# Kernel optimization log

Measured on AMD Instinct MI355X. Metric: run time of the kernel, lower is better.

The kernel has to match this reference:

```python
import jax, jax.numpy as jnp
import numpy as np

N = 50000          # total points (25 clouds x 2000 pts)
C = 64             # feature channels (in == out, no bottleneck)
K_NN = 16          # neighbors kept per dilation branch
DILATIONS = (1, 2, 4)
KMAX = K_NN * max(DILATIONS)   # base kNN graph has k*d_max neighbors per node
B = 25             # number of point clouds
EPS = 1e-16


def setup_inputs() -> dict:
    key = jax.random.key(0)
    ks = jax.random.split(key, 8)
    x = jax.random.normal(ks[0], (N, C), jnp.float32)
    pos = jax.random.normal(ks[1], (N, 3), jnp.float32)
    # kNN-style edge_index [2, N*KMAX]: row0 = source/neighbor j, row1 = center i,
    # KMAX consecutive edges per center node, neighbors restricted to the same cloud.
    pts = N // B
    cloud_base = (jnp.arange(N) // pts) * pts
    src = cloud_base[:, None] + jax.random.randint(ks[2], (N, KMAX), 0, pts)
    dst = jnp.broadcast_to(jnp.arange(N)[:, None], (N, KMAX))
    edge_index = jnp.stack([src.reshape(-1), dst.reshape(-1)]).astype(jnp.int32)
    batch = jnp.repeat(jnp.arange(B), pts).astype(jnp.int32)
    nD = len(DILATIONS)
    s = 1.0 / np.sqrt(C)
    Wv = jax.random.normal(ks[3], (nD, C, C), jnp.float32) * s   # lin (value)
    Wq = jax.random.normal(ks[4], (nD, C, C), jnp.float32) * s   # lin_dst
    Wk = jax.random.normal(ks[5], (nD, C, C), jnp.float32) * s   # lin_src
    Wp = jax.random.normal(ks[6], (nD, 3, C), jnp.float32) * (1.0 / np.sqrt(3.0))  # pos_nn
    bp = jax.random.normal(ks[7], (nD, C), jnp.float32) * 0.01
    return dict(x=x, pos=pos, Wv=Wv, Wq=Wq, Wk=Wk, Wp=Wp, bp=bp,
                edge_index=edge_index, batch=batch)


def _dilated_edges(edge_index, k, d):
    # take every d-th of the first k*d neighbors within each node's block -> k edges/node
    e = edge_index.reshape(2, -1, KMAX)[:, :, : k * d : d]
    return e.reshape(2, -1)


def _segment_softmax(a, seg, n):
    amax = jax.ops.segment_max(a, seg, num_segments=n)
    e = jnp.exp(a - amax[seg])
    s = jax.ops.segment_sum(e, seg, num_segments=n)
    return e / (s[seg] + EPS)


def _pt_conv(x, pos, src, dst, Wv, Wq, Wk, Wp, bp):
    # PyG PointTransformerConv: msg = softmax_i(q_i - k_j + delta_ij) * (v_j + delta_ij)
    n = x.shape[0]
    q = x @ Wq        # [N, C]  (lin_dst)
    kk = x @ Wk       # [N, C]  (lin_src)
    v = x @ Wv        # [N, C]  (lin, value)
    delta = (pos[dst] - pos[src]) @ Wp + bp            # [E, C] positional encoding
    alpha = _segment_softmax(q[dst] - kk[src] + delta, dst, n)
    return jax.ops.segment_sum(alpha * (v[src] + delta), dst, num_segments=n)


def reference(x, pos, Wv, Wq, Wk, Wp, bp, edge_index, batch):
    inputs = x
    res = None
    for i, d in enumerate(DILATIONS):
        e = _dilated_edges(edge_index, K_NN, d)
        h = _pt_conv(x, pos, e[0], e[1], Wv[i], Wq[i], Wk[i], Wp[i], bp[i])
        res = h if res is None else jnp.maximum(res, h)   # stack+max over branches
    # global max pool per cloud, gathered back per node
    pool = jax.ops.segment_max(x, batch, num_segments=B)[batch]
    res = jnp.maximum(res, pool)
    return res + inputs   # residual
```

## Files before the change

### kernel.cpp

```cpp
#include <hip/hip_runtime.h>
#include <math.h>

#define NP 50000
#define CH 64
#define KMAX 64
#define KNN 16
#define NB 25
#define PTS (NP / NB)
#define EPSF 1e-16f
#define NTILES (NP / 16)
#define ATILES (NP / 4)
#define L2E 1.4426950408889634f
#define LN2 0.6931471805599453f
#define PPB 8
#define PROWS (PTS / PPB)

typedef __attribute__((ext_vector_type(8))) short short8;
typedef __attribute__((ext_vector_type(4))) float float4v;
typedef __attribute__((ext_vector_type(4))) unsigned int uint4v;
typedef __attribute__((ext_vector_type(2))) unsigned int uint2v;
typedef __attribute__((ext_vector_type(4))) unsigned short ushort4v;

__device__ __forceinline__ ushort f2b(float f) {
  unsigned u = __float_as_uint(f);
  unsigned r = (u + 0x7FFFu + ((u >> 16) & 1u)) >> 16;
  return (ushort)r;
}
__device__ __forceinline__ float b2f(ushort h) {
  return __uint_as_float(((unsigned)h) << 16);
}

#define QBF_BYTES   ((size_t)3 * NP * CH * 2)
#define KVP_BYTES   ((size_t)3 * NP * CH * 4)
#define WPACK_ELEMS (9 * 4 * 2 * 64 * 8)

__global__ __launch_bounds__(256) void prep_kernel(
    const float* __restrict__ x,
    const float* __restrict__ Wv,
    const float* __restrict__ Wq,
    const float* __restrict__ Wk,
    ushort* __restrict__ wpack,
    float* __restrict__ poolP) {
  const int tid = threadIdx.x;
  const int bid = blockIdx.x;
  __shared__ float red[4][CH];

  if (bid < NB * PPB) {
    const int lane = tid & 63;
    const int wave = tid >> 6;
    const int cloud = bid >> 3;
    const int part  = bid & 7;
    const float* xb = x + ((size_t)cloud * PTS + part * PROWS) * CH;
    float m0 = -INFINITY, m1 = -INFINITY;
    for (int r = wave * 2; r < PROWS; r += 8) {
      m0 = fmaxf(m0, xb[(size_t)(r + 0) * CH + lane]);
      m1 = fmaxf(m1, xb[(size_t)(r + 1) * CH + lane]);
    }
    red[wave][lane] = fmaxf(m0, m1);
    __syncthreads();
    if (wave == 0) {
      poolP[(size_t)bid * CH + lane] = fmaxf(fmaxf(red[0][lane], red[1][lane]),
                                             fmaxf(red[2][lane], red[3][lane]));
    }
  } else {
    int pid = (bid - NB * PPB) * 256 + tid;
    if (pid < WPACK_ELEMS) {
      int j     = pid & 7;
      int lane  = (pid >> 3) & 63;
      int kstep = (pid >> 9) & 1;
      int mtile = (pid >> 10) & 3;
      int mat   = pid >> 12;
      const float* W;
      int d;
      float scale;
      if (mat < 3)      { W = Wq; d = mat;     scale = L2E; }
      else if (mat < 6) { W = Wk; d = mat - 3; scale = L2E; }
      else              { W = Wv; d = mat - 6; scale = 1.f; }
      int oc = mtile * 16 + (lane & 15);
      int ic = kstep * 32 + ((lane >> 4) & 3) * 8 + j;
      wpack[pid] = f2b(W[d * CH * CH + ic * CH + oc] * scale);
    }
  }
}

__global__ __launch_bounds__(384) void qkv_mfma(
    const float* __restrict__ x,
    const ushort* __restrict__ wpack,
    ushort* __restrict__ qbf,
    unsigned int* __restrict__ kvp) {
  const int tile = blockIdx.x;
  const int lane = threadIdx.x;
  const int wy   = threadIdx.y;
  const int tid  = wy * 64 + lane;

  __shared__ ushort xs[16 * 64];

  if (tid < 256) {
    int node  = tid >> 4;
    int chunk = tid & 15;
    float4v v = *(const float4v*)(x + ((size_t)(tile * 16 + node)) * CH + chunk * 4);
    ushort4v o;
    o[0] = f2b(v[0]); o[1] = f2b(v[1]); o[2] = f2b(v[2]); o[3] = f2b(v[3]);
    int byte = (chunk * 8) ^ ((node & 7) << 4);
    *(ushort4v*)((char*)xs + node * 128 + byte) = o;
  }
  __syncthreads();

  const int node = lane & 15;
  const int kb2  = (lane >> 4) * 16;
  const char* xrow = (const char*)xs + node * 128;
  const int sw = (node & 7) << 4;
  short8 b0 = *(const short8*)(xrow + (kb2 ^ sw));
  short8 b1 = *(const short8*)(xrow + ((kb2 + 64) ^ sw));
  const int myNode = tile * 16 + node;

  if (wy < 3) {
    const int dd = wy;
    ushort* outQ = qbf + (size_t)dd * NP * CH;
#pragma unroll
    for (int mt = 0; mt < 4; ++mt) {
      short8 a0 = *(const short8*)(wpack +
          ((((size_t)dd * 4 + mt) * 2 + 0) * 64 + lane) * 8);
      short8 a1 = *(const short8*)(wpack +
          ((((size_t)dd * 4 + mt) * 2 + 1) * 64 + lane) * 8);
      float4v acc = {0.f, 0.f, 0.f, 0.f};
      acc = __builtin_amdgcn_mfma_f32_16x16x32_bf16(a0, b0, acc, 0, 0, 0);
      acc = __builtin_amdgcn_mfma_f32_16x16x32_bf16(a1, b1, acc, 0, 0, 0);
      int oc = mt * 16 + (lane >> 4) * 4;
      uint2v o;
      o[0] = (unsigned)f2b(acc[0]) | ((unsigned)f2b(acc[1]) << 16);
      o[1] = (unsigned)f2b(acc[2]) | ((unsigned)f2b(acc[3]) << 16);
      *(uint2v*)(outQ + (size_t)myNode * CH + oc) = o;
    }
  } else {
    const int dd = wy - 3;
    unsigned int* outKV = kvp + (size_t)dd * NP * CH;
#pragma unroll
    for (int mt = 0; mt < 4; ++mt) {
      short8 k0 = *(const short8*)(wpack +
          ((((size_t)(3 + dd) * 4 + mt) * 2 + 0) * 64 + lane) * 8);
      short8 k1 = *(const short8*)(wpack +
          ((((size_t)(3 + dd) * 4 + mt) * 2 + 1) * 64 + lane) * 8);
      short8 v0 = *(const short8*)(wpack +
          ((((size_t)(6 + dd) * 4 + mt) * 2 + 0) * 64 + lane) * 8);
      short8 v1 = *(const short8*)(wpack +
          ((((size_t)(6 + dd) * 4 + mt) * 2 + 1) * 64 + lane) * 8);
      float4v aK = {0.f, 0.f, 0.f, 0.f};
      float4v aV = {0.f, 0.f, 0.f, 0.f};
      aK = __builtin_amdgcn_mfma_f32_16x16x32_bf16(k0, b0, aK, 0, 0, 0);
      aK = __builtin_amdgcn_mfma_f32_16x16x32_bf16(k1, b1, aK, 0, 0, 0);
      aV = __builtin_amdgcn_mfma_f32_16x16x32_bf16(v0, b0, aV, 0, 0, 0);
      aV = __builtin_amdgcn_mfma_f32_16x16x32_bf16(v1, b1, aV, 0, 0, 0);
      int oc = mt * 16 + (lane >> 4) * 4;
      uint4v o;
#pragma unroll
      for (int i = 0; i < 4; ++i)
        o[i] = ((unsigned)f2b(aK[i]) << 16) | (unsigned)f2b(aV[i]);
      *(uint4v*)(outKV + (size_t)myNode * CH + oc) = o;
    }
  }
}

__global__ __launch_bounds__(384, 6) void attn_kernel(
    const float* __restrict__ x,
    const float* __restrict__ pos,
    const float* __restrict__ Wp,
    const float* __restrict__ bp,
    const int*   __restrict__ edge_src,
    const ushort* __restrict__ qbf,
    const unsigned int* __restrict__ kvp,
    const float* __restrict__ poolP,
    float* __restrict__ out) {
  const int bx  = blockIdx.x;
  const int xcd = bx & 7;
  const int kk  = bx >> 3;
  const int base = (ATILES * xcd) >> 3;
  const int cnt  = ((ATILES * (xcd + 1)) >> 3) - base;
  if (kk >= cnt) return;
  const int node0 = (base + kk) * 4;

  const int wy   = threadIdx.y;
  const int dd   = wy % 3;
  const int half = wy / 3;
  const int tid  = wy * 64 + threadIdx.x;

  __shared__ float sEdge[4 * 260];
  __shared__ float sS[6 * 4 * 68];
  __shared__ float sP[6 * 4 * 68];

  if (tid < 256) {
    int nl = tid >> 6, p = tid & 63;
    int nd = node0 + nl;
    int j = edge_src[(size_t)nd * KMAX + p];
    float4v w;
    w[0] = pos[nd * 3 + 0] - pos[j * 3 + 0];
    w[1] = pos[nd * 3 + 1] - pos[j * 3 + 1];
    w[2] = pos[nd * 3 + 2] - pos[j * 3 + 2];
    w[3] = __int_as_float(j << 8);
    *(float4v*)&sEdge[nl * 260 + p * 4] = w;
  }
  __syncthreads();

  const int lane = threadIdx.x;
  const int g    = lane >> 4;
  const int cl   = lane & 15;
  const int node = node0 + g;
  const unsigned clOfs = (unsigned)(cl << 4);

  float4v bq, qorig, wp0, wp1, wp2;
  {
    ushort4v qh = *(const ushort4v*)(qbf + ((size_t)dd * NP + node) * CH + cl * 4);
    const float* WpD = Wp + dd * 192;
    wp0 = *(const float4v*)(WpD + 0 * 64 + cl * 4) * L2E;
    wp1 = *(const float4v*)(WpD + 1 * 64 + cl * 4) * L2E;
    wp2 = *(const float4v*)(WpD + 2 * 64 + cl * 4) * L2E;
    float4v bpv = *(const float4v*)(bp + dd * 64 + cl * 4);
    float4v qf;
#pragma unroll
    for (int i = 0; i < 4; ++i) qf[i] = b2f(qh[i]);
    bq = qf + bpv * L2E;
    qorig = qf * LN2;
  }
  const char* KVb = (const char*)(kvp + (size_t)dd * NP * CH);

  const float* ep = &sEdge[g * 260] + (((half * 8) << dd) * 4);
  const int estep = (1 << dd) * 4;

  float4v s    = {0.f, 0.f, 0.f, 0.f};
  float4v accv = {0.f, 0.f, 0.f, 0.f};
#pragma unroll
  for (int e = 0; e < 8; ++e) {
    float4v w = *(const float4v*)ep;
    ep += estep;
    uint4v u = *(const uint4v*)(KVb + (__float_as_uint(w[3]) + clOfs));
    float4v kf, vf, wgt;
#pragma unroll
    for (int i = 0; i < 4; ++i) kf[i] = __uint_as_float(u[i] & 0xFFFF0000u);
#pragma unroll
    for (int i = 0; i < 4; ++i) vf[i] = __uint_as_float(u[i] << 16);
    float4v t = bq + w[0] * wp0 + w[1] * wp1 + w[2] * wp2;
    float4v a = t - kf;
#pragma unroll
    for (int i = 0; i < 4; ++i) wgt[i] = __builtin_amdgcn_exp2f(a[i]);
    s += wgt;
    accv += wgt * (vf + t * LN2);
  }

  float4v P = accv - qorig * s;
  *(float4v*)&sS[(wy * 4 + g) * 68 + cl * 4] = s;
  *(float4v*)&sP[(wy * 4 + g) * 68 + cl * 4] = P;
  __syncthreads();

  if (wy == 0) {
    float4v res;
#pragma unroll
    for (int d2 = 0; d2 < 3; ++d2) {
      float4v s0 = *(const float4v*)&sS[((d2    ) * 4 + g) * 68 + cl * 4];
      float4v s1 = *(const float4v*)&sS[((d2 + 3) * 4 + g) * 68 + cl * 4];
      float4v p0 = *(const float4v*)&sP[((d2    ) * 4 + g) * 68 + cl * 4];
      float4v p1 = *(const float4v*)&sP[((d2 + 3) * 4 + g) * 68 + cl * 4];
      float4v st = s0 + s1;
      float4v pt = p0 + p1;
      float4v r;
#pragma unroll
      for (int i = 0; i < 4; ++i)
        r[i] = pt[i] * __builtin_amdgcn_rcpf(st[i] + EPSF);
      if (d2 == 0) res = r;
      else {
#pragma unroll
        for (int i = 0; i < 4; ++i) res[i] = fmaxf(res[i], r[i]);
      }
    }
    const int b = node / PTS;
    const float* pp = poolP + (size_t)(b * PPB) * CH + cl * 4;
    float4v pv = *(const float4v*)pp;
#pragma unroll
    for (int q2 = 1; q2 < PPB; ++q2) {
      float4v t2 = *(const float4v*)(pp + (size_t)q2 * CH);
#pragma unroll
      for (int i = 0; i < 4; ++i) pv[i] = fmaxf(pv[i], t2[i]);
    }
    float4v xv = *(const float4v*)(x + (size_t)node * CH + cl * 4);
#pragma unroll
    for (int i = 0; i < 4; ++i) res[i] = fmaxf(res[i], pv[i]) + xv[i];
    *(float4v*)(out + (size_t)node * CH + cl * 4) = res;
  }
}

extern "C" void kernel_launch(void* const* d_in, const int* in_sizes, int n_in,
                              void* d_out, int out_size, void* d_ws, size_t ws_size,
                              hipStream_t stream) {
  const float* x    = (const float*)d_in[0];
  const float* pos  = (const float*)d_in[1];
  const float* Wv   = (const float*)d_in[2];
  const float* Wq   = (const float*)d_in[3];
  const float* Wk   = (const float*)d_in[4];
  const float* Wp   = (const float*)d_in[5];
  const float* bp   = (const float*)d_in[6];
  const int*   ei   = (const int*)d_in[7];
  float* out = (float*)d_out;

  char* wsb = (char*)d_ws;
  ushort* qbf   = (ushort*)wsb;
  unsigned int* kvp = (unsigned int*)(wsb + QBF_BYTES);
  ushort* wpack = (ushort*)(wsb + QBF_BYTES + KVP_BYTES);
  float*  poolP = (float*)(wsb + QBF_BYTES + KVP_BYTES +
                           (size_t)WPACK_ELEMS * 2);

  {
    int packBlocks = (WPACK_ELEMS + 255) / 256;
    dim3 grid(NB * PPB + packBlocks);
    hipLaunchKernelGGL(prep_kernel, grid, dim3(256), 0, stream,
                       x, Wv, Wq, Wk, wpack, poolP);
  }
  {
    dim3 grid(NTILES);
    dim3 block(64, 6);
    hipLaunchKernelGGL(qkv_mfma, grid, block, 0, stream, x, wpack, qbf, kvp);
  }
  {
    dim3 grid(8 * ((ATILES + 7) / 8));
    dim3 block(64, 6);
    hipLaunchKernelGGL(attn_kernel, grid, block, 0, stream,
                       x, pos, Wp, bp, ei, qbf, kvp, poolP, out);
  }
}
```

Measured before the change: 191.1 us.

## Gather only used neighbor edges, prefetch pool/residual early, XCD-remap QKV tiles

The attention kernel now loads only the 48 dilated neighbor edges each node actually uses, instead of all 64, into a compacted shared layout, so the edge-loop reads become contiguous. The pool-max and residual loads move before the first barrier on the finalizing wave (wave 5), so their latency overlaps with the edge gather. The QKV GEMM grid is remapped so that contiguous tiles land on the same XCD, matching the attention kernel. This adds index arithmetic and pads the grid slightly.

```diff
diff --git a/kernel.cpp b/kernel.cpp
--- a/kernel.cpp
+++ b/kernel.cpp
@@ -88,7 +88,14 @@
     const ushort* __restrict__ wpack,
     ushort* __restrict__ qbf,
     unsigned int* __restrict__ kvp) {
-  const int tile = blockIdx.x;
+  const int bx  = blockIdx.x;
+  const int xcd = bx & 7;
+  const int kk  = bx >> 3;
+  const int tbase = (NTILES * xcd) >> 3;
+  const int tcnt  = ((NTILES * (xcd + 1)) >> 3) - tbase;
+  if (kk >= tcnt) return;
+  const int tile = tbase + kk;
+
   const int lane = threadIdx.x;
   const int wy   = threadIdx.y;
   const int tid  = wy * 64 + lane;
@@ -181,32 +188,16 @@
 
   const int wy   = threadIdx.y;
   const int dd   = wy % 3;
-  const int half = wy / 3;
-  const int tid  = wy * 64 + threadIdx.x;
-
-  __shared__ float sEdge[4 * 260];
-  __shared__ float sS[6 * 4 * 68];
-  __shared__ float sP[6 * 4 * 68];
-
-  if (tid < 256) {
-    int nl = tid >> 6, p = tid & 63;
-    int nd = node0 + nl;
-    int j = edge_src[(size_t)nd * KMAX + p];
-    float4v w;
-    w[0] = pos[nd * 3 + 0] - pos[j * 3 + 0];
-    w[1] = pos[nd * 3 + 1] - pos[j * 3 + 1];
-    w[2] = pos[nd * 3 + 2] - pos[j * 3 + 2];
-    w[3] = __int_as_float(j << 8);
-    *(float4v*)&sEdge[nl * 260 + p * 4] = w;
-  }
-  __syncthreads();
-
   const int lane = threadIdx.x;
   const int g    = lane >> 4;
   const int cl   = lane & 15;
   const int node = node0 + g;
+
+  __shared__ float sEdge[4 * 196];
+  __shared__ float sS[6 * 4 * 68];
+  __shared__ float sP[6 * 4 * 68];
+
   const unsigned clOfs = (unsigned)(cl << 4);
-
   float4v bq, qorig, wp0, wp1, wp2;
   {
     ushort4v qh = *(const ushort4v*)(qbf + ((size_t)dd * NP + node) * CH + cl * 4);
@@ -221,17 +212,45 @@
     bq = qf + bpv * L2E;
     qorig = qf * LN2;
   }
+
+  float4v pvmax = {0.f, 0.f, 0.f, 0.f};
+  float4v xres  = {0.f, 0.f, 0.f, 0.f};
+  if (wy == 5) {
+    const int b = node0 / PTS;
+    const float* pp = poolP + (size_t)(b * PPB) * CH + cl * 4;
+    pvmax = *(const float4v*)pp;
+#pragma unroll
+    for (int q2 = 1; q2 < PPB; ++q2) {
+      float4v t2 = *(const float4v*)(pp + (size_t)q2 * CH);
+#pragma unroll
+      for (int i = 0; i < 4; ++i) pvmax[i] = fmaxf(pvmax[i], t2[i]);
+    }
+    xres = *(const float4v*)(x + (size_t)node * CH + cl * 4);
+  }
+
+  if (wy < 4 && lane < 48) {
+    int wv = lane >> 3, e = lane & 7;
+    int dds = wv >= 3 ? wv - 3 : wv;
+    int p = (wv >= 3 ? (8 << dds) : 0) + (e << dds);
+    int nd = node0 + wy;
+    int j = edge_src[(size_t)nd * KMAX + p];
+    float4v w;
+    w[0] = pos[nd * 3 + 0] - pos[j * 3 + 0];
+    w[1] = pos[nd * 3 + 1] - pos[j * 3 + 1];
+    w[2] = pos[nd * 3 + 2] - pos[j * 3 + 2];
+    w[3] = __int_as_float(j << 8);
+    *(float4v*)&sEdge[wy * 196 + lane * 4] = w;
+  }
+  __syncthreads();
+
   const char* KVb = (const char*)(kvp + (size_t)dd * NP * CH);
-
-  const float* ep = &sEdge[g * 260] + (((half * 8) << dd) * 4);
-  const int estep = (1 << dd) * 4;
+  const float* ep = &sEdge[g * 196 + wy * 32];
 
   float4v s    = {0.f, 0.f, 0.f, 0.f};
   float4v accv = {0.f, 0.f, 0.f, 0.f};
 #pragma unroll
   for (int e = 0; e < 8; ++e) {
-    float4v w = *(const float4v*)ep;
-    ep += estep;
+    float4v w = *(const float4v*)(ep + e * 4);
     uint4v u = *(const uint4v*)(KVb + (__float_as_uint(w[3]) + clOfs));
     float4v kf, vf, wgt;
 #pragma unroll
@@ -251,7 +270,7 @@
   *(float4v*)&sP[(wy * 4 + g) * 68 + cl * 4] = P;
   __syncthreads();
 
-  if (wy == 0) {
+  if (wy == 5) {
     float4v res;
 #pragma unroll
     for (int d2 = 0; d2 < 3; ++d2) {
@@ -271,18 +290,8 @@
         for (int i = 0; i < 4; ++i) res[i] = fmaxf(res[i], r[i]);
       }
     }
-    const int b = node / PTS;
-    const float* pp = poolP + (size_t)(b * PPB) * CH + cl * 4;
-    float4v pv = *(const float4v*)pp;
-#pragma unroll
-    for (int q2 = 1; q2 < PPB; ++q2) {
-      float4v t2 = *(const float4v*)(pp + (size_t)q2 * CH);
-#pragma unroll
-      for (int i = 0; i < 4; ++i) pv[i] = fmaxf(pv[i], t2[i]);
-    }
-    float4v xv = *(const float4v*)(x + (size_t)node * CH + cl * 4);
-#pragma unroll
-    for (int i = 0; i < 4; ++i) res[i] = fmaxf(res[i], pv[i]) + xv[i];
+#pragma unroll
+    for (int i = 0; i < 4; ++i) res[i] = fmaxf(res[i], pvmax[i]) + xres[i];
     *(float4v*)(out + (size_t)node * CH + cl * 4) = res;
   }
 }
@@ -314,7 +323,7 @@
                        x, Wv, Wq, Wk, wpack, poolP);
   }
   {
-    dim3 grid(NTILES);
+    dim3 grid(8 * ((NTILES + 7) / 8));
     dim3 block(64, 6);
     hipLaunchKernelGGL(qkv_mfma, grid, block, 0, stream, x, wpack, qbf, kvp);
   }
```

Result: slower. 196.5 us (+2.8%).
